# Performance work log

Measured on AMD Instinct MI355X. Metric: run time of the kernel, lower is better.

Reference implementation:

```python
import jax, jax.numpy as jnp
import numpy as np

N, E, G = 20000, 320000, 128
H, TE, CD = 128, 128, 64
HEADS, DH = 4, 32          # inner = 128 == H
L = 6


def _fwd(p, edge_index, batch):
    """Faithful forward of CrystalDiffusionModel (eval mode: dropout = identity).
    EquivariantGraphConv (imported in the original) is implemented as the standard
    edge-conditioned message-passing conv: m_ij = silu(W[h_src; h_dst; e_ij] + b),
    agg = scatter_add over dst, h' = W_u[h; agg] + b_u."""
    x, ea, t = p['x'], p['edge_attr'], p['t']
    n = x.shape[0]
    h = x @ p['Wn'] + p['bn']                      # [N,H] node embedding
    ef = ea @ p['We'] + p['be']                    # [E,H] edge embedding

    # sinusoidal time embedding -> MLP
    half = TE // 2
    freq = jnp.exp(-jnp.arange(half, dtype=jnp.float32) * (np.log(10000.0) / (half - 1)))
    te = t[:, None] * freq[None, :]
    te = jnp.concatenate([jnp.sin(te), jnp.cos(te)], axis=-1)          # [G,TE]
    te = jax.nn.silu(te @ p['tm_W1'] + p['tm_b1']) @ p['tm_W2'] + p['tm_b2']

    def mlp2(z, W1, b1, W2, b2):
        return jax.nn.silu(z @ W1 + b1) @ W2 + b2

    topo_e = mlp2(p['topo_cond'], p['topo_W1'], p['topo_b1'], p['topo_W2'], p['topo_b2'])
    stab_e = mlp2(p['stab_cond'], p['stab_W1'], p['stab_b1'], p['stab_W2'], p['stab_b2'])
    sust_e = mlp2(p['sust_cond'], p['sust_W1'], p['sust_b1'], p['sust_W2'], p['sust_b2'])
    cond = mlp2(jnp.concatenate([topo_e, stab_e, sust_e], axis=-1),
                p['comb_W1'], p['comb_b1'], p['comb_W2'], p['comb_b2'])  # [G,CD]

    ctx = cond[batch]                               # [N,CD] per-node condition
    # context is a single token per query -> k,v constant across layers
    k = (ctx @ p['Wk']).reshape(n, HEADS, DH)
    v = (ctx @ p['Wv']).reshape(n, HEADS, DH)
    ti = jax.nn.silu(te)[batch]                     # [N,H] time influence (dropout=id)

    src, dst = edge_index[0], edge_index[1]
    scale = DH ** -0.5
    for i in range(L):
        Wm, bm = p['gnn_Wm'][i], p['gnn_bm'][i]
        # split concat-GEMM to avoid materializing [E, 3H]
        m = jax.nn.silu(h[src] @ Wm[:H] + h[dst] @ Wm[H:2 * H] + ef @ Wm[2 * H:] + bm)
        agg = jax.ops.segment_sum(m, dst, num_segments=n)               # [N,H]
        Wu, bu = p['gnn_Wu'][i], p['gnn_bu'][i]
        hu = h @ Wu[:H] + agg @ Wu[H:] + bu
        # LayerNorm
        mu = hu.mean(-1, keepdims=True)
        var = hu.var(-1, keepdims=True)
        hu = (hu - mu) * jax.lax.rsqrt(var + 1e-5) * p['ln_g'][i] + p['ln_b'][i]
        # cross-attention; context length is 1 so softmax over j is exactly 1
        q = (hu @ p['Wq']).reshape(n, HEADS, DH)
        sim = jnp.einsum('nhd,nhd->nh', q, k) * scale                   # [N,heads]
        attn = jax.nn.softmax(sim[..., None], axis=-1)                  # == 1.0
        out = (attn * v).reshape(n, HEADS * DH)
        hu = out @ p['Wo'] + p['bo']
        h = h + hu + ti                              # residual + time influence

    node_pred = jax.nn.silu(h @ p['np_W1'] + p['np_b1']) @ p['np_W2'] + p['np_b2']
    pos_pred = jax.nn.silu(h @ p['pp_W1'] + p['pp_b1']) @ p['pp_W2'] + p['pp_b2']
    return node_pred, pos_pred


def setup_inputs() -> dict:
    key = jax.random.key(0)
    it = iter(jax.random.split(key, 96))

    def nrm(shape, s=0.02):
        return jax.random.normal(next(it), shape, jnp.float32) * s

    z = lambda *s: jnp.zeros(s, jnp.float32)
    inp = {
        'x': jax.random.normal(next(it), (N, 12), jnp.float32),
        'edge_index': jax.random.randint(next(it), (2, E), 0, N),
        'edge_attr': jax.random.normal(next(it), (E, 20), jnp.float32),
        'pos': jax.random.normal(next(it), (N, 3), jnp.float32),
        't': jax.random.uniform(next(it), (G,), jnp.float32) * 1000.0,
        'topo_cond': jax.random.normal(next(it), (G, 7), jnp.float32),
        'stab_cond': jax.random.normal(next(it), (G, 2), jnp.float32),
        'sust_cond': jax.random.normal(next(it), (G, 3), jnp.float32),
        'batch': jnp.sort(jax.random.randint(next(it), (N,), 0, G)),
        'Wn': nrm((12, H)), 'bn': z(H), 'We': nrm((20, H)), 'be': z(H),
        'tm_W1': nrm((TE, 2 * TE)), 'tm_b1': z(2 * TE), 'tm_W2': nrm((2 * TE, TE)), 'tm_b2': z(TE),
        'topo_W1': nrm((7, 32)), 'topo_b1': z(32), 'topo_W2': nrm((32, 32)), 'topo_b2': z(32),
        'stab_W1': nrm((2, 16)), 'stab_b1': z(16), 'stab_W2': nrm((16, 16)), 'stab_b2': z(16),
        'sust_W1': nrm((3, 16)), 'sust_b1': z(16), 'sust_W2': nrm((16, 16)), 'sust_b2': z(16),
        'comb_W1': nrm((64, CD)), 'comb_b1': z(CD), 'comb_W2': nrm((CD, CD)), 'comb_b2': z(CD),
        'Wq': nrm((H, HEADS * DH)), 'Wk': nrm((CD, HEADS * DH)), 'Wv': nrm((CD, HEADS * DH)),
        'Wo': nrm((HEADS * DH, H)), 'bo': z(H),
        'gnn_Wm': nrm((L, 3 * H, H)), 'gnn_bm': z(L, H),
        'gnn_Wu': nrm((L, 2 * H, H)), 'gnn_bu': z(L, H),
        'ln_g': jnp.ones((L, H), jnp.float32), 'ln_b': z(L, H),
        'np_W1': nrm((H, 2 * H)), 'np_b1': z(2 * H), 'np_W2': nrm((2 * H, 12)), 'np_b2': z(12),
        'pp_W1': nrm((H, H)), 'pp_b1': z(H), 'pp_W2': nrm((H, 3)), 'pp_b2': z(3),
    }
    return inp


def reference(x, edge_index, edge_attr, pos, t, topo_cond, stab_cond, sust_cond, batch,
              Wn, bn, We, be, tm_W1, tm_b1, tm_W2, tm_b2,
              topo_W1, topo_b1, topo_W2, topo_b2, stab_W1, stab_b1, stab_W2, stab_b2,
              sust_W1, sust_b1, sust_W2, sust_b2, comb_W1, comb_b1, comb_W2, comb_b2,
              Wq, Wk, Wv, Wo, bo, gnn_Wm, gnn_bm, gnn_Wu, gnn_bu, ln_g, ln_b,
              np_W1, np_b1, np_W2, np_b2, pp_W1, pp_b1, pp_W2, pp_b2):
    loc = dict(locals())
    p = {k: v for k, v in loc.items() if k not in ('edge_index', 'batch', 'pos')}
    return _fwd(p, edge_index, batch)
```

## Files before the change

### kernel.cpp

```cpp
#include <hip/hip_runtime.h>
#include <hip/hip_bf16.h>

#define NN 20000
#define GG 128
#define BN 64

typedef __bf16 bf16x8_t __attribute__((ext_vector_type(8)));
typedef float  f32x4_t  __attribute__((ext_vector_type(4)));
typedef __hip_bfloat16 hbf16;

#define PK_NPW1 32768
#define PK_PPW1 65536
#define PK_NPW2 81920
#define PK_PPW2 86016

__device__ __forceinline__ float silu_f(float v) {
    return v / (1.0f + expf(-v));
}

__global__ __launch_bounds__(256) void graph_kernel(
        const float* __restrict__ t, const float* __restrict__ topo,
        const float* __restrict__ stab, const float* __restrict__ sust,
        const float* __restrict__ tmW1, const float* __restrict__ tmb1,
        const float* __restrict__ tmW2, const float* __restrict__ tmb2,
        const float* __restrict__ topoW1, const float* __restrict__ topob1,
        const float* __restrict__ topoW2, const float* __restrict__ topob2,
        const float* __restrict__ stabW1, const float* __restrict__ stabb1,
        const float* __restrict__ stabW2, const float* __restrict__ stabb2,
        const float* __restrict__ sustW1, const float* __restrict__ sustb1,
        const float* __restrict__ sustW2, const float* __restrict__ sustb2,
        const float* __restrict__ combW1, const float* __restrict__ combb1,
        const float* __restrict__ combW2, const float* __restrict__ combb2,
        const float* __restrict__ Wv, const float* __restrict__ Wo,
        const float* __restrict__ bo,
        const float* __restrict__ npW1, const float* __restrict__ npW2,
        const float* __restrict__ ppW1, const float* __restrict__ ppW2,
        float* __restrict__ gadd, hbf16* __restrict__ wsb) {
    __shared__ float s_te[128];
    __shared__ float s_th1[256];
    __shared__ float s_tef[128];
    __shared__ float s_l1[64];
    __shared__ float s_cat[64];
    __shared__ float s_c1[64];
    __shared__ float s_cond[64];
    __shared__ float s_v[128];
    __shared__ float s_red[256];

    const int g = blockIdx.x;
    const int tid = threadIdx.x;

    {
        int s0 = blockIdx.x * 256 + tid;
#pragma unroll
        for (int e = 0; e < 2; ++e) {
            int s = s0 + e * 32768;
            if (s < 32768) {
                const int p = s;
                const int j = p & 7, l = (p >> 3) & 63, kb = (p >> 9) & 3, ct = p >> 11;
                const int k = kb * 32 + ((l >> 4) << 3) + j;
                const int n = ct * 16 + (l & 15);
                wsb[PK_NPW1 + p] = __float2bfloat16(npW1[k * 256 + n]);
            } else if (s < 49152) {
                const int p = s - 32768;
                const int j = p & 7, l = (p >> 3) & 63, kb = (p >> 9) & 3, ct = p >> 11;
                const int k = kb * 32 + ((l >> 4) << 3) + j;
                const int n = ct * 16 + (l & 15);
                wsb[PK_PPW1 + p] = __float2bfloat16(ppW1[k * 128 + n]);
            } else if (s < 53248) {
                const int p = s - 49152;
                const int j = p & 7, l = (p >> 3) & 63, kb = p >> 9;
                const int k = kb * 32 + ((l >> 4) << 3) + j;
                const int n = l & 15;
                wsb[PK_NPW2 + p] = __float2bfloat16(n < 12 ? npW2[k * 12 + n] : 0.0f);
            } else if (s < 55296) {
                const int p = s - 53248;
                const int j = p & 7, l = (p >> 3) & 63, kb = p >> 9;
                const int k = kb * 32 + ((l >> 4) << 3) + j;
                const int n = l & 15;
                wsb[PK_PPW2 + p] = __float2bfloat16(n < 3 ? ppW2[k * 3 + n] : 0.0f);
            }
        }
    }

    if (tid < 128) {
        const float tval = t[g];
        const int i = tid & 63;
        const float fr = expf(-(float)i * 0.14619587892025688f);
        const float arg = tval * fr;
        s_te[tid] = (tid < 64) ? sinf(arg) : cosf(arg);
    } else if (tid < 192) {
        const int c = tid - 128;
        if (c < 32) {
            float acc = topob1[c];
            for (int k = 0; k < 7; ++k)
                acc += topo[g * 7 + k] * topoW1[k * 32 + c];
            s_l1[c] = silu_f(acc);
        } else if (c < 48) {
            const int j = c - 32;
            float acc = stabb1[j];
            for (int k = 0; k < 2; ++k)
                acc += stab[g * 2 + k] * stabW1[k * 16 + j];
            s_l1[c] = silu_f(acc);
        } else {
            const int j = c - 48;
            float acc = sustb1[j];
            for (int k = 0; k < 3; ++k)
                acc += sust[g * 3 + k] * sustW1[k * 16 + j];
            s_l1[c] = silu_f(acc);
        }
    }
    __syncthreads();

    {
        float acc = tmb1[tid];
#pragma unroll 4
        for (int k = 0; k < 128; ++k)
            acc += s_te[k] * tmW1[k * 256 + tid];
        s_th1[tid] = silu_f(acc);
    }
    __syncthreads();

    {
        const int j = tid & 127, half = tid >> 7;
        float acc = 0.0f;
#pragma unroll 4
        for (int kk = 0; kk < 128; ++kk)
            acc += s_th1[half * 128 + kk] * tmW2[(half * 128 + kk) * 128 + j];
        s_red[tid] = acc;
    }
    __syncthreads();

    if (tid < 128) {
        s_tef[tid] = tmb2[tid] + s_red[tid] + s_red[tid + 128];
    } else if (tid < 192) {
        const int c = tid - 128;
        if (c < 32) {
            float acc = topob2[c];
            for (int k = 0; k < 32; ++k)
                acc += s_l1[k] * topoW2[k * 32 + c];
            s_cat[c] = acc;
        } else if (c < 48) {
            const int j = c - 32;
            float acc = stabb2[j];
            for (int k = 0; k < 16; ++k)
                acc += s_l1[32 + k] * stabW2[k * 16 + j];
            s_cat[c] = acc;
        } else {
            const int j = c - 48;
            float acc = sustb2[j];
            for (int k = 0; k < 16; ++k)
                acc += s_l1[48 + k] * sustW2[k * 16 + j];
            s_cat[c] = acc;
        }
    }
    __syncthreads();

    {
        const int j = tid & 63, part = tid >> 6;
        float acc = 0.0f;
#pragma unroll
        for (int kk = 0; kk < 16; ++kk)
            acc += s_cat[part * 16 + kk] * combW1[(part * 16 + kk) * 64 + j];
        s_red[tid] = acc;
    }
    __syncthreads();
    if (tid < 64)
        s_c1[tid] = silu_f(combb1[tid] + s_red[tid] + s_red[tid + 64] +
                           s_red[tid + 128] + s_red[tid + 192]);
    __syncthreads();

    {
        const int j = tid & 63, part = tid >> 6;
        float acc = 0.0f;
#pragma unroll
        for (int kk = 0; kk < 16; ++kk)
            acc += s_c1[part * 16 + kk] * combW2[(part * 16 + kk) * 64 + j];
        s_red[tid] = acc;
    }
    __syncthreads();
    if (tid < 64)
        s_cond[tid] = combb2[tid] + s_red[tid] + s_red[tid + 64] +
                      s_red[tid + 128] + s_red[tid + 192];
    __syncthreads();

    {
        const int j = tid & 127, half = tid >> 7;
        float acc = 0.0f;
#pragma unroll
        for (int kk = 0; kk < 32; ++kk)
            acc += s_cond[half * 32 + kk] * Wv[(half * 32 + kk) * 128 + j];
        s_red[tid] = acc;
    }
    __syncthreads();
    if (tid < 128) s_v[tid] = s_red[tid] + s_red[tid + 128];
    __syncthreads();

    {
        const int j = tid & 127, half = tid >> 7;
        float acc = 0.0f;
#pragma unroll 4
        for (int kk = 0; kk < 64; ++kk)
            acc += s_v[half * 64 + kk] * Wo[(half * 64 + kk) * 128 + j];
        s_red[tid] = acc;
    }
    __syncthreads();
    if (tid < 128)
        gadd[g * 128 + tid] =
            6.0f * (bo[tid] + s_red[tid] + s_red[tid + 128] + silu_f(s_tef[tid]));
}

__global__ __launch_bounds__(256) void node_kernel(
        const float* __restrict__ x, const int* __restrict__ batch,
        const float* __restrict__ Wn, const float* __restrict__ bn,
        const float* __restrict__ npb1, const float* __restrict__ npb2,
        const float* __restrict__ ppb1, const float* __restrict__ ppb2,
        const float* __restrict__ gadd, const hbf16* __restrict__ wsb,
        float* __restrict__ out) {
    __shared__ __align__(16) hbf16 hA[BN * 136];
    __shared__ __align__(16) hbf16 zs[BN * 264];

    const int nb = blockIdx.x * BN;
    const int tid = threadIdx.x;
    const int lane = tid & 63;
    const int w = tid >> 6;
    const int q = lane >> 4;
    const int r = lane & 15;

    for (int idx = tid; idx < BN * 128; idx += 256) {
        const int nl = idx >> 7;
        const int d  = idx & 127;
        const int gn = nb + nl;
        float acc = 0.0f;
        if (gn < NN) {
            const int b = batch[gn];
            acc = bn[d] + gadd[b * 128 + d];
#pragma unroll
            for (int k = 0; k < 12; ++k)
                acc += x[gn * 12 + k] * Wn[k * 128 + d];
        }
        hA[nl * 136 + d] = __float2bfloat16(acc);
    }
    __syncthreads();

    {
        f32x4_t acc[4][4];
#pragma unroll
        for (int ci = 0; ci < 4; ++ci)
#pragma unroll
            for (int rt = 0; rt < 4; ++rt) acc[ci][rt] = (f32x4_t){0.f, 0.f, 0.f, 0.f};

        for (int kb = 0; kb < 4; ++kb) {
            bf16x8_t Af[4];
#pragma unroll
            for (int rt = 0; rt < 4; ++rt)
                Af[rt] = *reinterpret_cast<const bf16x8_t*>(
                    &hA[(rt * 16 + r) * 136 + kb * 32 + q * 8]);
#pragma unroll
            for (int ci = 0; ci < 4; ++ci) {
                const int ct = w * 4 + ci;
                bf16x8_t Bf = *reinterpret_cast<const bf16x8_t*>(
                    &wsb[PK_NPW1 + ((ct * 4 + kb) * 64 + lane) * 8]);
#pragma unroll
                for (int rt = 0; rt < 4; ++rt)
                    acc[ci][rt] = __builtin_amdgcn_mfma_f32_16x16x32_bf16(
                        Af[rt], Bf, acc[ci][rt], 0, 0, 0);
            }
        }
#pragma unroll
        for (int ci = 0; ci < 4; ++ci) {
            const int col = (w * 4 + ci) * 16 + r;
            const float b1 = npb1[col];
#pragma unroll
            for (int rt = 0; rt < 4; ++rt) {
#pragma unroll
                for (int i = 0; i < 4; ++i) {
                    const int m = rt * 16 + q * 4 + i;
                    zs[m * 264 + col] = __float2bfloat16(silu_f(acc[ci][rt][i] + b1));
                }
            }
        }
    }
    __syncthreads();

    {
        f32x4_t acc2 = (f32x4_t){0.f, 0.f, 0.f, 0.f};
        for (int kb = 0; kb < 8; ++kb) {
            bf16x8_t Af = *reinterpret_cast<const bf16x8_t*>(
                &zs[(w * 16 + r) * 264 + kb * 32 + q * 8]);
            bf16x8_t Bf = *reinterpret_cast<const bf16x8_t*>(
                &wsb[PK_NPW2 + (kb * 64 + lane) * 8]);
            acc2 = __builtin_amdgcn_mfma_f32_16x16x32_bf16(Af, Bf, acc2, 0, 0, 0);
        }
        if (r < 12) {
            const float b2 = npb2[r];
#pragma unroll
            for (int i = 0; i < 4; ++i) {
                const int gn = nb + w * 16 + q * 4 + i;
                if (gn < NN) out[gn * 12 + r] = acc2[i] + b2;
            }
        }
    }
    __syncthreads();

    {
        f32x4_t acc[2][4];
#pragma unroll
        for (int ci = 0; ci < 2; ++ci)
#pragma unroll
            for (int rt = 0; rt < 4; ++rt) acc[ci][rt] = (f32x4_t){0.f, 0.f, 0.f, 0.f};

        for (int kb = 0; kb < 4; ++kb) {
            bf16x8_t Af[4];
#pragma unroll
            for (int rt = 0; rt < 4; ++rt)
                Af[rt] = *reinterpret_cast<const bf16x8_t*>(
                    &hA[(rt * 16 + r) * 136 + kb * 32 + q * 8]);
#pragma unroll
            for (int ci = 0; ci < 2; ++ci) {
                const int ct = w * 2 + ci;
                bf16x8_t Bf = *reinterpret_cast<const bf16x8_t*>(
                    &wsb[PK_PPW1 + ((ct * 4 + kb) * 64 + lane) * 8]);
#pragma unroll
                for (int rt = 0; rt < 4; ++rt)
                    acc[ci][rt] = __builtin_amdgcn_mfma_f32_16x16x32_bf16(
                        Af[rt], Bf, acc[ci][rt], 0, 0, 0);
            }
        }
        __syncthreads();
#pragma unroll
        for (int ci = 0; ci < 2; ++ci) {
            const int col = (w * 2 + ci) * 16 + r;
            const float b1 = ppb1[col];
#pragma unroll
            for (int rt = 0; rt < 4; ++rt) {
#pragma unroll
                for (int i = 0; i < 4; ++i) {
                    const int m = rt * 16 + q * 4 + i;
                    zs[m * 136 + col] = __float2bfloat16(silu_f(acc[ci][rt][i] + b1));
                }
            }
        }
    }
    __syncthreads();

    {
        f32x4_t acc2 = (f32x4_t){0.f, 0.f, 0.f, 0.f};
        for (int kb = 0; kb < 4; ++kb) {
            bf16x8_t Af = *reinterpret_cast<const bf16x8_t*>(
                &zs[(w * 16 + r) * 136 + kb * 32 + q * 8]);
            bf16x8_t Bf = *reinterpret_cast<const bf16x8_t*>(
                &wsb[PK_PPW2 + (kb * 64 + lane) * 8]);
            acc2 = __builtin_amdgcn_mfma_f32_16x16x32_bf16(Af, Bf, acc2, 0, 0, 0);
        }
        if (r < 3) {
            const float b2 = ppb2[r];
#pragma unroll
            for (int i = 0; i < 4; ++i) {
                const int gn = nb + w * 16 + q * 4 + i;
                if (gn < NN) out[NN * 12 + gn * 3 + r] = acc2[i] + b2;
            }
        }
    }
}

extern "C" void kernel_launch(void* const* d_in, const int* in_sizes, int n_in,
                              void* d_out, int out_size, void* d_ws, size_t ws_size,
                              hipStream_t stream) {
    const float* x      = (const float*)d_in[0];
    const float* t      = (const float*)d_in[4];
    const float* topo   = (const float*)d_in[5];
    const float* stab   = (const float*)d_in[6];
    const float* sust   = (const float*)d_in[7];
    const int*   batch  = (const int*)d_in[8];
    const float* Wn     = (const float*)d_in[9];
    const float* bn     = (const float*)d_in[10];
    const float* tmW1   = (const float*)d_in[13];
    const float* tmb1   = (const float*)d_in[14];
    const float* tmW2   = (const float*)d_in[15];
    const float* tmb2   = (const float*)d_in[16];
    const float* topoW1 = (const float*)d_in[17];
    const float* topob1 = (const float*)d_in[18];
    const float* topoW2 = (const float*)d_in[19];
    const float* topob2 = (const float*)d_in[20];
    const float* stabW1 = (const float*)d_in[21];
    const float* stabb1 = (const float*)d_in[22];
    const float* stabW2 = (const float*)d_in[23];
    const float* stabb2 = (const float*)d_in[24];
    const float* sustW1 = (const float*)d_in[25];
    const float* sustb1 = (const float*)d_in[26];
    const float* sustW2 = (const float*)d_in[27];
    const float* sustb2 = (const float*)d_in[28];
    const float* combW1 = (const float*)d_in[29];
    const float* combb1 = (const float*)d_in[30];
    const float* combW2 = (const float*)d_in[31];
    const float* combb2 = (const float*)d_in[32];
    const float* Wv     = (const float*)d_in[35];
    const float* Wo     = (const float*)d_in[36];
    const float* bo     = (const float*)d_in[37];
    const float* npW1   = (const float*)d_in[44];
    const float* npb1   = (const float*)d_in[45];
    const float* npW2   = (const float*)d_in[46];
    const float* npb2   = (const float*)d_in[47];
    const float* ppW1   = (const float*)d_in[48];
    const float* ppb1   = (const float*)d_in[49];
    const float* ppW2   = (const float*)d_in[50];
    const float* ppb2   = (const float*)d_in[51];

    float* gadd = (float*)d_ws;
    hbf16* wsb  = (hbf16*)d_ws;
    float* out  = (float*)d_out;

    graph_kernel<<<GG, 256, 0, stream>>>(t, topo, stab, sust,
                                         tmW1, tmb1, tmW2, tmb2,
                                         topoW1, topob1, topoW2, topob2,
                                         stabW1, stabb1, stabW2, stabb2,
                                         sustW1, sustb1, sustW2, sustb2,
                                         combW1, combb1, combW2, combb2,
                                         Wv, Wo, bo,
                                         npW1, npW2, ppW1, ppW2,
                                         gadd, wsb);

    node_kernel<<<(NN + BN - 1) / BN, 256, 0, stream>>>(
        x, batch, Wn, bn, npb1, npb2, ppb1, ppb2, gadd, wsb, out);
}
```

Measured before the change: 234.2 us.

## Make node MLP wave-private, compute node embedding with MFMA and drop block barriers

The node kernel is restructured so each wavefront owns 16 nodes end to end and computes all output columns itself, so the block-wide __syncthreads calls go away. The x@Wn node embedding now runs as an MFMA over a bf16-packed, zero-padded Wn that graph_kernel prepares. The intent is to cut barrier stalls and the scalar FMA loop. In exchange each wave loads every weight fragment itself rather than sharing them across the block, register pressure rises (launch_bounds set to 256,1), and x is rounded to bf16 before the embedding.

```diff
diff --git a/kernel.cpp b/kernel.cpp
--- a/kernel.cpp
+++ b/kernel.cpp
@@ -3,7 +3,6 @@
 
 #define NN 20000
 #define GG 128
-#define BN 64
 
 typedef __bf16 bf16x8_t __attribute__((ext_vector_type(8)));
 typedef float  f32x4_t  __attribute__((ext_vector_type(4)));
@@ -13,6 +12,7 @@
 #define PK_PPW1 65536
 #define PK_NPW2 81920
 #define PK_PPW2 86016
+#define PK_WN   88064
 
 __device__ __forceinline__ float silu_f(float v) {
     return v / (1.0f + expf(-v));
@@ -35,6 +35,7 @@
         const float* __restrict__ bo,
         const float* __restrict__ npW1, const float* __restrict__ npW2,
         const float* __restrict__ ppW1, const float* __restrict__ ppW2,
+        const float* __restrict__ Wn,
         float* __restrict__ gadd, hbf16* __restrict__ wsb) {
     __shared__ float s_te[128];
     __shared__ float s_th1[256];
@@ -50,10 +51,9 @@
     const int tid = threadIdx.x;
 
     {
-        int s0 = blockIdx.x * 256 + tid;
 #pragma unroll
         for (int e = 0; e < 2; ++e) {
-            int s = s0 + e * 32768;
+            const int s = blockIdx.x * 512 + e * 256 + tid;
             if (s < 32768) {
                 const int p = s;
                 const int j = p & 7, l = (p >> 3) & 63, kb = (p >> 9) & 3, ct = p >> 11;
@@ -78,6 +78,12 @@
                 const int k = kb * 32 + ((l >> 4) << 3) + j;
                 const int n = l & 15;
                 wsb[PK_PPW2 + p] = __float2bfloat16(n < 3 ? ppW2[k * 3 + n] : 0.0f);
+            } else if (s < 59392) {
+                const int p = s - 55296;
+                const int j = p & 7, l = (p >> 3) & 63, ct = p >> 9;
+                const int k = ((l >> 4) << 3) + j;
+                const int n = ct * 16 + (l & 15);
+                wsb[PK_WN + p] = __float2bfloat16(k < 12 ? Wn[k * 128 + n] : 0.0f);
             }
         }
     }
@@ -209,85 +215,114 @@
             6.0f * (bo[tid] + s_red[tid] + s_red[tid + 128] + silu_f(s_tef[tid]));
 }
 
-__global__ __launch_bounds__(256) void node_kernel(
+__global__ __launch_bounds__(256, 1) void node_kernel(
         const float* __restrict__ x, const int* __restrict__ batch,
-        const float* __restrict__ Wn, const float* __restrict__ bn,
+        const float* __restrict__ bn,
         const float* __restrict__ npb1, const float* __restrict__ npb2,
         const float* __restrict__ ppb1, const float* __restrict__ ppb2,
         const float* __restrict__ gadd, const hbf16* __restrict__ wsb,
         float* __restrict__ out) {
-    __shared__ __align__(16) hbf16 hA[BN * 136];
-    __shared__ __align__(16) hbf16 zs[BN * 264];
-
-    const int nb = blockIdx.x * BN;
-    const int tid = threadIdx.x;
+    __shared__ __align__(16) hbf16 z1s[4 * 16 * 264];
+    __shared__ __align__(16) hbf16 hs[4 * 16 * 136];
+
+    const int tid  = threadIdx.x;
+    const int w    = tid >> 6;
     const int lane = tid & 63;
-    const int w = tid >> 6;
-    const int q = lane >> 4;
-    const int r = lane & 15;
-
-    for (int idx = tid; idx < BN * 128; idx += 256) {
-        const int nl = idx >> 7;
-        const int d  = idx & 127;
-        const int gn = nb + nl;
-        float acc = 0.0f;
-        if (gn < NN) {
-            const int b = batch[gn];
-            acc = bn[d] + gadd[b * 128 + d];
-#pragma unroll
-            for (int k = 0; k < 12; ++k)
-                acc += x[gn * 12 + k] * Wn[k * 128 + d];
-        }
-        hA[nl * 136 + d] = __float2bfloat16(acc);
-    }
-    __syncthreads();
-
-    {
-        f32x4_t acc[4][4];
-#pragma unroll
-        for (int ci = 0; ci < 4; ++ci)
-#pragma unroll
-            for (int rt = 0; rt < 4; ++rt) acc[ci][rt] = (f32x4_t){0.f, 0.f, 0.f, 0.f};
-
+    const int q    = lane >> 4;
+    const int r    = lane & 15;
+    const int n16  = blockIdx.x * 64 + w * 16;
+
+    hbf16* wz1 = z1s + w * (16 * 264);
+    hbf16* wh  = hs  + w * (16 * 136);
+
+    bf16x8_t Ax;
+    {
+        const int node = n16 + r;
+        float xv[8];
+#pragma unroll
+        for (int j = 0; j < 8; ++j) xv[j] = 0.0f;
+        if (node < NN) {
+            if (q == 0) {
+                const float4 a = *reinterpret_cast<const float4*>(x + node * 12);
+                const float4 b = *reinterpret_cast<const float4*>(x + node * 12 + 4);
+                xv[0] = a.x; xv[1] = a.y; xv[2] = a.z; xv[3] = a.w;
+                xv[4] = b.x; xv[5] = b.y; xv[6] = b.z; xv[7] = b.w;
+            } else if (q == 1) {
+                const float4 a = *reinterpret_cast<const float4*>(x + node * 12 + 8);
+                xv[0] = a.x; xv[1] = a.y; xv[2] = a.z; xv[3] = a.w;
+            }
+        }
+#pragma unroll
+        for (int j = 0; j < 8; ++j) {
+            const hbf16 tv = __float2bfloat16(xv[j]);
+            Ax[j] = *reinterpret_cast<const __bf16*>(&tv);
+        }
+    }
+
+    int bidx[4];
+#pragma unroll
+    for (int i = 0; i < 4; ++i) {
+        const int gn = n16 + q * 4 + i;
+        bidx[i] = (gn < NN) ? batch[gn] : 0;
+    }
+
+    f32x4_t hacc[8];
+#pragma unroll
+    for (int ct = 0; ct < 8; ++ct) {
+        const bf16x8_t Bf = *reinterpret_cast<const bf16x8_t*>(
+            &wsb[PK_WN + (ct * 64 + lane) * 8]);
+        hacc[ct] = __builtin_amdgcn_mfma_f32_16x16x32_bf16(
+            Ax, Bf, (f32x4_t){0.f, 0.f, 0.f, 0.f}, 0, 0, 0);
+    }
+#pragma unroll
+    for (int ct = 0; ct < 8; ++ct) {
+        const int n = ct * 16 + r;
+        const float bv = bn[n];
+#pragma unroll
+        for (int i = 0; i < 4; ++i) {
+            const float hv = hacc[ct][i] + bv + gadd[bidx[i] * 128 + n];
+            wh[(q * 4 + i) * 136 + n] = __float2bfloat16(hv);
+        }
+    }
+
+    bf16x8_t Ah[4];
+#pragma unroll
+    for (int kb = 0; kb < 4; ++kb)
+        Ah[kb] = *reinterpret_cast<const bf16x8_t*>(
+            &wh[r * 136 + kb * 32 + q * 8]);
+
+    {
+        f32x4_t acc[16];
+#pragma unroll
+        for (int ct = 0; ct < 16; ++ct) acc[ct] = (f32x4_t){0.f, 0.f, 0.f, 0.f};
+#pragma unroll
         for (int kb = 0; kb < 4; ++kb) {
-            bf16x8_t Af[4];
-#pragma unroll
-            for (int rt = 0; rt < 4; ++rt)
-                Af[rt] = *reinterpret_cast<const bf16x8_t*>(
-                    &hA[(rt * 16 + r) * 136 + kb * 32 + q * 8]);
-#pragma unroll
-            for (int ci = 0; ci < 4; ++ci) {
-                const int ct = w * 4 + ci;
-                bf16x8_t Bf = *reinterpret_cast<const bf16x8_t*>(
+#pragma unroll
+            for (int ct = 0; ct < 16; ++ct) {
+                const bf16x8_t Bf = *reinterpret_cast<const bf16x8_t*>(
                     &wsb[PK_NPW1 + ((ct * 4 + kb) * 64 + lane) * 8]);
-#pragma unroll
-                for (int rt = 0; rt < 4; ++rt)
-                    acc[ci][rt] = __builtin_amdgcn_mfma_f32_16x16x32_bf16(
-                        Af[rt], Bf, acc[ci][rt], 0, 0, 0);
-            }
-        }
-#pragma unroll
-        for (int ci = 0; ci < 4; ++ci) {
-            const int col = (w * 4 + ci) * 16 + r;
+                acc[ct] = __builtin_amdgcn_mfma_f32_16x16x32_bf16(
+                    Ah[kb], Bf, acc[ct], 0, 0, 0);
+            }
+        }
+#pragma unroll
+        for (int ct = 0; ct < 16; ++ct) {
+            const int col = ct * 16 + r;
             const float b1 = npb1[col];
 #pragma unroll
-            for (int rt = 0; rt < 4; ++rt) {
-#pragma unroll
-                for (int i = 0; i < 4; ++i) {
-                    const int m = rt * 16 + q * 4 + i;
-                    zs[m * 264 + col] = __float2bfloat16(silu_f(acc[ci][rt][i] + b1));
-                }
-            }
-        }
-    }
-    __syncthreads();
+            for (int i = 0; i < 4; ++i)
+                wz1[(q * 4 + i) * 264 + col] =
+                    __float2bfloat16(silu_f(acc[ct][i] + b1));
+        }
+    }
 
     {
         f32x4_t acc2 = (f32x4_t){0.f, 0.f, 0.f, 0.f};
+#pragma unroll
         for (int kb = 0; kb < 8; ++kb) {
-            bf16x8_t Af = *reinterpret_cast<const bf16x8_t*>(
-                &zs[(w * 16 + r) * 264 + kb * 32 + q * 8]);
-            bf16x8_t Bf = *reinterpret_cast<const bf16x8_t*>(
+            const bf16x8_t Af = *reinterpret_cast<const bf16x8_t*>(
+                &wz1[r * 264 + kb * 32 + q * 8]);
+            const bf16x8_t Bf = *reinterpret_cast<const bf16x8_t*>(
                 &wsb[PK_NPW2 + (kb * 64 + lane) * 8]);
             acc2 = __builtin_amdgcn_mfma_f32_16x16x32_bf16(Af, Bf, acc2, 0, 0, 0);
         }
@@ -295,60 +330,44 @@
             const float b2 = npb2[r];
 #pragma unroll
             for (int i = 0; i < 4; ++i) {
-                const int gn = nb + w * 16 + q * 4 + i;
+                const int gn = n16 + q * 4 + i;
                 if (gn < NN) out[gn * 12 + r] = acc2[i] + b2;
             }
         }
     }
-    __syncthreads();
-
-    {
-        f32x4_t acc[2][4];
-#pragma unroll
-        for (int ci = 0; ci < 2; ++ci)
-#pragma unroll
-            for (int rt = 0; rt < 4; ++rt) acc[ci][rt] = (f32x4_t){0.f, 0.f, 0.f, 0.f};
-
+
+    {
+        f32x4_t acc[8];
+#pragma unroll
+        for (int ct = 0; ct < 8; ++ct) acc[ct] = (f32x4_t){0.f, 0.f, 0.f, 0.f};
+#pragma unroll
         for (int kb = 0; kb < 4; ++kb) {
-            bf16x8_t Af[4];
-#pragma unroll
-            for (int rt = 0; rt < 4; ++rt)
-                Af[rt] = *reinterpret_cast<const bf16x8_t*>(
-                    &hA[(rt * 16 + r) * 136 + kb * 32 + q * 8]);
-#pragma unroll
-            for (int ci = 0; ci < 2; ++ci) {
-                const int ct = w * 2 + ci;
-                bf16x8_t Bf = *reinterpret_cast<const bf16x8_t*>(
+#pragma unroll
+            for (int ct = 0; ct < 8; ++ct) {
+                const bf16x8_t Bf = *reinterpret_cast<const bf16x8_t*>(
                     &wsb[PK_PPW1 + ((ct * 4 + kb) * 64 + lane) * 8]);
-#pragma unroll
-                for (int rt = 0; rt < 4; ++rt)
-                    acc[ci][rt] = __builtin_amdgcn_mfma_f32_16x16x32_bf16(
-                        Af[rt], Bf, acc[ci][rt], 0, 0, 0);
-            }
-        }
-        __syncthreads();
-#pragma unroll
-        for (int ci = 0; ci < 2; ++ci) {
-            const int col = (w * 2 + ci) * 16 + r;
+                acc[ct] = __builtin_amdgcn_mfma_f32_16x16x32_bf16(
+                    Ah[kb], Bf, acc[ct], 0, 0, 0);
+            }
+        }
+#pragma unroll
+        for (int ct = 0; ct < 8; ++ct) {
+            const int col = ct * 16 + r;
             const float b1 = ppb1[col];
 #pragma unroll
-            for (int rt = 0; rt < 4; ++rt) {
-#pragma unroll
-                for (int i = 0; i < 4; ++i) {
-                    const int m = rt * 16 + q * 4 + i;
-                    zs[m * 136 + col] = __float2bfloat16(silu_f(acc[ci][rt][i] + b1));
-                }
-            }
-        }
-    }
-    __syncthreads();
+            for (int i = 0; i < 4; ++i)
+                wh[(q * 4 + i) * 136 + col] =
+                    __float2bfloat16(silu_f(acc[ct][i] + b1));
+        }
+    }
 
     {
         f32x4_t acc2 = (f32x4_t){0.f, 0.f, 0.f, 0.f};
+#pragma unroll
         for (int kb = 0; kb < 4; ++kb) {
-            bf16x8_t Af = *reinterpret_cast<const bf16x8_t*>(
-                &zs[(w * 16 + r) * 136 + kb * 32 + q * 8]);
-            bf16x8_t Bf = *reinterpret_cast<const bf16x8_t*>(
+            const bf16x8_t Af = *reinterpret_cast<const bf16x8_t*>(
+                &wh[r * 136 + kb * 32 + q * 8]);
+            const bf16x8_t Bf = *reinterpret_cast<const bf16x8_t*>(
                 &wsb[PK_PPW2 + (kb * 64 + lane) * 8]);
             acc2 = __builtin_amdgcn_mfma_f32_16x16x32_bf16(Af, Bf, acc2, 0, 0, 0);
         }
@@ -356,7 +375,7 @@
             const float b2 = ppb2[r];
 #pragma unroll
             for (int i = 0; i < 4; ++i) {
-                const int gn = nb + w * 16 + q * 4 + i;
+                const int gn = n16 + q * 4 + i;
                 if (gn < NN) out[NN * 12 + gn * 3 + r] = acc2[i] + b2;
             }
         }
@@ -417,9 +436,9 @@
                                          sustW1, sustb1, sustW2, sustb2,
                                          combW1, combb1, combW2, combb2,
                                          Wv, Wo, bo,
-                                         npW1, npW2, ppW1, ppW2,
+                                         npW1, npW2, ppW1, ppW2, Wn,
                                          gadd, wsb);
 
-    node_kernel<<<(NN + BN - 1) / BN, 256, 0, stream>>>(
-        x, batch, Wn, bn, npb1, npb2, ppb1, ppb2, gadd, wsb, out);
+    node_kernel<<<(NN + 63) / 64, 256, 0, stream>>>(
+        x, batch, bn, npb1, npb2, ppb1, ppb2, gadd, wsb, out);
 }
```

Result: no change. 232.6 us (-0.7%).
